# Kernel tuning notes

Hardware: AMD Instinct MI355X
Metric: run time of the kernel (lower is better)

## Reference

```python
import jax, jax.numpy as jnp
import numpy as np

B, N, IN_DIM, OUT_DIM, K = 64, 256, 512, 512, 8
DK = OUT_DIM // K  # per-kernel feature dim


def setup_inputs() -> dict:
    key = jax.random.key(0)
    k1, k2, k3, k4 = jax.random.split(key, 4)
    node_feats = jax.random.normal(k1, (B, N, IN_DIM), dtype=jnp.float32)
    adj = jax.random.uniform(k2, (B, K, N, N), dtype=jnp.float32)
    weight = jax.random.normal(k3, (IN_DIM, OUT_DIM), dtype=jnp.float32) * (1.0 / np.sqrt(IN_DIM))
    bias = jax.random.normal(k4, (OUT_DIM,), dtype=jnp.float32) * 0.01
    return {"node_feats": node_feats, "adj": adj, "weight": weight, "bias": bias}


def reference(node_feats, adj, weight, bias):
    # kernel linear + ReLU: (b, n, out_dim)
    h = jax.nn.relu(jnp.einsum('bni,io->bno', node_feats, weight) + bias)
    # split into kernel slots: (b, n, k, dk)
    h = h.reshape(B, N, K, DK)
    # graph.aggregate: per-kernel dense message passing over adjacency
    # out[b,n,k,d] = sum_m adj[b,k,n,m] * h[b,m,k,d]
    agg = jnp.einsum('bknm,bmkd->bnkd', adj, h)
    return agg.reshape(B, N, OUT_DIM)
```

## Files before the change

### kernel.cpp

```cpp
#include <hip/hip_runtime.h>
#include <hip/hip_bf16.h>


typedef __attribute__((ext_vector_type(8))) short short8;
typedef __attribute__((ext_vector_type(4))) float floatx4;

__device__ __forceinline__ unsigned short f2bf(float f) {
    union { float f; unsigned u; } v; v.f = f;
    unsigned r = v.u + 0x7FFFu + ((v.u >> 16) & 1u);
    return (unsigned short)(r >> 16);
}

__global__ __launch_bounds__(256) void wt_kernel(const float* __restrict__ W,
                                                 unsigned short* __restrict__ Wt) {
    int idx = blockIdx.x * 256 + threadIdx.x;
    int k = idx >> 9;
    int o = idx & 511;
    Wt[o * 512 + k] = f2bf(W[idx]);
}

__global__ __launch_bounds__(256) void gemm_relu_kernel(
    const float* __restrict__ X, const unsigned short* __restrict__ Wt,
    const float* __restrict__ bias, unsigned short* __restrict__ hT) {
    __shared__ unsigned short a_lds[128 * 40];
    __shared__ unsigned short b_lds[128 * 40];

    const int tid = threadIdx.x;
    const int lane = tid & 63, wid = tid >> 6;
    const int wm = (wid & 1) * 64, wn = (wid >> 1) * 64;
    const int lrow = lane & 15, quad = lane >> 4;
    const int m_base = blockIdx.x * 128;
    const int o_base = blockIdx.y * 128;

    floatx4 acc[4][4];
    const floatx4 fzero = {0.f, 0.f, 0.f, 0.f};
#pragma unroll
    for (int i = 0; i < 4; ++i)
#pragma unroll
        for (int j = 0; j < 4; ++j) acc[i][j] = fzero;

    for (int kb = 0; kb < 16; ++kb) {
        const int k0 = kb * 32;
#pragma unroll
        for (int i = 0; i < 4; ++i) {
            int c4 = tid + i * 256;
            int r = c4 >> 3;
            int cc = (c4 & 7) * 4;
            const float4 v = *(const float4*)(X + (size_t)(m_base + r) * 512 + k0 + cc);
            ushort4 p;
            p.x = f2bf(v.x); p.y = f2bf(v.y); p.z = f2bf(v.z); p.w = f2bf(v.w);
            *(ushort4*)(a_lds + r * 40 + cc) = p;
        }
#pragma unroll
        for (int i = 0; i < 4; ++i) {
            int c4 = tid + i * 256;
            int r = c4 >> 3;
            int cc = (c4 & 7) * 4;
            *(ushort4*)(b_lds + r * 40 + cc) =
                *(const ushort4*)(Wt + (size_t)(o_base + r) * 512 + k0 + cc);
        }
        __syncthreads();

        short8 af[4], bfr[4];
#pragma unroll
        for (int i = 0; i < 4; ++i)
            af[i] = *(const short8*)(a_lds + (wm + 16 * i + lrow) * 40 + quad * 8);
#pragma unroll
        for (int j = 0; j < 4; ++j)
            bfr[j] = *(const short8*)(b_lds + (wn + 16 * j + lrow) * 40 + quad * 8);
#pragma unroll
        for (int i = 0; i < 4; ++i)
#pragma unroll
            for (int j = 0; j < 4; ++j)
                acc[i][j] = __builtin_amdgcn_mfma_f32_16x16x32_bf16(af[i], bfr[j], acc[i][j], 0, 0, 0);
        __syncthreads();
    }

    const int b = blockIdx.x >> 1;
    const int m_in_b = (blockIdx.x & 1) * 128;
#pragma unroll
    for (int j = 0; j < 4; ++j) {
        int o = o_base + wn + 16 * j + lrow;
        float bv = bias[o];
        int ks = o >> 6, d = o & 63;
        unsigned short* dst = hT + ((size_t)(b * 8 + ks) * 64 + d) * 256;
#pragma unroll
        for (int i = 0; i < 4; ++i) {
            int m = m_in_b + wm + 16 * i + quad * 4;
            floatx4 c = acc[i][j];
            ushort4 p;
            p.x = f2bf(fmaxf(c.x + bv, 0.f));
            p.y = f2bf(fmaxf(c.y + bv, 0.f));
            p.z = f2bf(fmaxf(c.z + bv, 0.f));
            p.w = f2bf(fmaxf(c.w + bv, 0.f));
            *(ushort4*)(dst + m) = p;
        }
    }
}

__global__ __launch_bounds__(256) void agg_kernel(const float* __restrict__ adj,
                                                  const unsigned short* __restrict__ hT,
                                                  float* __restrict__ out) {
    const int tid = threadIdx.x;
    const int lane = tid & 63, wid = tid >> 6;
    const int bk = blockIdx.x >> 1;
    const int half = blockIdx.x & 1;
    const int b = bk >> 3, ks = bk & 7;
    const int lrow = lane & 15, quad = lane >> 4;
    const int n0 = half * 128 + wid * 32;

    const float* A = adj + (size_t)bk * 65536;
    const unsigned short* Bh = hT + (size_t)bk * 16384;

    floatx4 acc[2][4];
    const floatx4 fzero = {0.f, 0.f, 0.f, 0.f};
#pragma unroll
    for (int i = 0; i < 2; ++i)
#pragma unroll
        for (int j = 0; j < 4; ++j) acc[i][j] = fzero;

    for (int mt = 0; mt < 8; ++mt) {
        const int m0 = mt * 32 + quad * 8;
        short8 af[2], bfr[4];
#pragma unroll
        for (int i = 0; i < 2; ++i) {
            const float* src = A + (size_t)(n0 + 16 * i + lrow) * 256 + m0;
            float4 v0 = *(const float4*)src;
            float4 v1 = *(const float4*)(src + 4);
            short8 t;
            t[0] = (short)f2bf(v0.x); t[1] = (short)f2bf(v0.y);
            t[2] = (short)f2bf(v0.z); t[3] = (short)f2bf(v0.w);
            t[4] = (short)f2bf(v1.x); t[5] = (short)f2bf(v1.y);
            t[6] = (short)f2bf(v1.z); t[7] = (short)f2bf(v1.w);
            af[i] = t;
        }
#pragma unroll
        for (int j = 0; j < 4; ++j)
            bfr[j] = *(const short8*)(Bh + (16 * j + lrow) * 256 + m0);
#pragma unroll
        for (int i = 0; i < 2; ++i)
#pragma unroll
            for (int j = 0; j < 4; ++j)
                acc[i][j] = __builtin_amdgcn_mfma_f32_16x16x32_bf16(af[i], bfr[j], acc[i][j], 0, 0, 0);
    }

#pragma unroll
    for (int i = 0; i < 2; ++i) {
#pragma unroll
        for (int j = 0; j < 4; ++j) {
            int n = n0 + 16 * i + quad * 4;
            int d = 16 * j + lrow;
            float* dst = out + ((size_t)b * 256 + n) * 512 + ks * 64 + d;
            floatx4 c = acc[i][j];
            dst[0 * 512] = c.x;
            dst[1 * 512] = c.y;
            dst[2 * 512] = c.z;
            dst[3 * 512] = c.w;
        }
    }
}

extern "C" void kernel_launch(void* const* d_in, const int* in_sizes, int n_in,
                              void* d_out, int out_size, void* d_ws, size_t ws_size,
                              hipStream_t stream) {
    const float* X    = (const float*)d_in[0];
    const float* adj  = (const float*)d_in[1];
    const float* W    = (const float*)d_in[2];
    const float* bias = (const float*)d_in[3];
    float* out = (float*)d_out;

    unsigned short* hT = (unsigned short*)d_ws;
    unsigned short* Wt = hT + (size_t)64 * 8 * 64 * 256;

    wt_kernel<<<1024, 256, 0, stream>>>(W, Wt);
    gemm_relu_kernel<<<dim3(128, 4), 256, 0, stream>>>(X, Wt, bias, hT);
    agg_kernel<<<1024, 256, 0, stream>>>(adj, hT, out);
}
```

Measured before the change: 260.6 us.

## Tile weight transpose via LDS, use packed bf16 conversion, remap block order

The weight transpose kernel now stages 64x64 tiles through padded shared memory, so both its global reads and its writes are coalesced. Float-to-bf16 conversion switches to the packed __float22bfloat162_rn intrinsic in all kernels. The gemm and agg kernels remap block IDs so that consecutive groups of eight blocks take different m-tiles or bk slices, which changes how work spreads across XCDs and caches. The agg kernel reads a large fp32 adjacency tensor and likely dominates runtime, so these changes mostly touch the smaller stages.

```diff
diff --git a/kernel.cpp b/kernel.cpp
--- a/kernel.cpp
+++ b/kernel.cpp
@@ -11,12 +11,32 @@
     return (unsigned short)(r >> 16);
 }
 
+__device__ __forceinline__ unsigned pk2bf(float a, float b) {
+    union { __hip_bfloat162 h; unsigned u; } cv;
+    cv.h = __float22bfloat162_rn(make_float2(a, b));
+    return cv.u;
+}
+
 __global__ __launch_bounds__(256) void wt_kernel(const float* __restrict__ W,
                                                  unsigned short* __restrict__ Wt) {
-    int idx = blockIdx.x * 256 + threadIdx.x;
-    int k = idx >> 9;
-    int o = idx & 511;
-    Wt[o * 512 + k] = f2bf(W[idx]);
+    __shared__ unsigned short t_lds[64 * 66];
+    const int tile = blockIdx.x;
+    const int k0 = (tile >> 3) * 64;
+    const int o0 = (tile & 7) * 64;
+    const int t = threadIdx.x;
+    const int c = t & 63;
+    const int rb = t >> 6;
+#pragma unroll
+    for (int i = 0; i < 16; ++i) {
+        int r = i * 4 + rb;
+        t_lds[c * 66 + r] = f2bf(W[(size_t)(k0 + r) * 512 + o0 + c]);
+    }
+    __syncthreads();
+#pragma unroll
+    for (int i = 0; i < 16; ++i) {
+        int o_r = i * 4 + rb;
+        Wt[(size_t)(o0 + o_r) * 512 + k0 + c] = t_lds[o_r * 66 + c];
+    }
 }
 
 __global__ __launch_bounds__(256) void gemm_relu_kernel(
@@ -25,12 +45,18 @@
     __shared__ unsigned short a_lds[128 * 40];
     __shared__ unsigned short b_lds[128 * 40];
 
+    const int id = blockIdx.x;
+    const int r8 = id & 7;
+    const int yt = (id >> 3) & 3;
+    const int q  = id >> 5;
+    const int m_tile = r8 + 8 * q;
+    const int m_base = m_tile * 128;
+    const int o_base = yt * 128;
+
     const int tid = threadIdx.x;
     const int lane = tid & 63, wid = tid >> 6;
     const int wm = (wid & 1) * 64, wn = (wid >> 1) * 64;
     const int lrow = lane & 15, quad = lane >> 4;
-    const int m_base = blockIdx.x * 128;
-    const int o_base = blockIdx.y * 128;
 
     floatx4 acc[4][4];
     const floatx4 fzero = {0.f, 0.f, 0.f, 0.f};
@@ -44,20 +70,21 @@
 #pragma unroll
         for (int i = 0; i < 4; ++i) {
             int c4 = tid + i * 256;
-            int r = c4 >> 3;
+            int rr = c4 >> 3;
             int cc = (c4 & 7) * 4;
-            const float4 v = *(const float4*)(X + (size_t)(m_base + r) * 512 + k0 + cc);
-            ushort4 p;
-            p.x = f2bf(v.x); p.y = f2bf(v.y); p.z = f2bf(v.z); p.w = f2bf(v.w);
-            *(ushort4*)(a_lds + r * 40 + cc) = p;
+            const float4 v = *(const float4*)(X + (size_t)(m_base + rr) * 512 + k0 + cc);
+            unsigned p01 = pk2bf(v.x, v.y);
+            unsigned p23 = pk2bf(v.z, v.w);
+            unsigned* dst = (unsigned*)(a_lds + rr * 40 + cc);
+            dst[0] = p01; dst[1] = p23;
         }
 #pragma unroll
         for (int i = 0; i < 4; ++i) {
             int c4 = tid + i * 256;
-            int r = c4 >> 3;
+            int rr = c4 >> 3;
             int cc = (c4 & 7) * 4;
-            *(ushort4*)(b_lds + r * 40 + cc) =
-                *(const ushort4*)(Wt + (size_t)(o_base + r) * 512 + k0 + cc);
+            *(ushort4*)(b_lds + rr * 40 + cc) =
+                *(const ushort4*)(Wt + (size_t)(o_base + rr) * 512 + k0 + cc);
         }
         __syncthreads();
 
@@ -76,8 +103,8 @@
         __syncthreads();
     }
 
-    const int b = blockIdx.x >> 1;
-    const int m_in_b = (blockIdx.x & 1) * 128;
+    const int b = m_tile >> 1;
+    const int m_in_b = (m_tile & 1) * 128;
 #pragma unroll
     for (int j = 0; j < 4; ++j) {
         int o = o_base + wn + 16 * j + lrow;
@@ -88,12 +115,10 @@
         for (int i = 0; i < 4; ++i) {
             int m = m_in_b + wm + 16 * i + quad * 4;
             floatx4 c = acc[i][j];
-            ushort4 p;
-            p.x = f2bf(fmaxf(c.x + bv, 0.f));
-            p.y = f2bf(fmaxf(c.y + bv, 0.f));
-            p.z = f2bf(fmaxf(c.z + bv, 0.f));
-            p.w = f2bf(fmaxf(c.w + bv, 0.f));
-            *(ushort4*)(dst + m) = p;
+            unsigned p01 = pk2bf(fmaxf(c.x + bv, 0.f), fmaxf(c.y + bv, 0.f));
+            unsigned p23 = pk2bf(fmaxf(c.z + bv, 0.f), fmaxf(c.w + bv, 0.f));
+            unsigned* d32 = (unsigned*)(dst + m);
+            d32[0] = p01; d32[1] = p23;
         }
     }
 }
@@ -101,10 +126,14 @@
 __global__ __launch_bounds__(256) void agg_kernel(const float* __restrict__ adj,
                                                   const unsigned short* __restrict__ hT,
                                                   float* __restrict__ out) {
+    const int id = blockIdx.x;
+    const int r8 = id & 7;
+    const int half = (id >> 3) & 1;
+    const int q = id >> 4;
+    const int bk = r8 + 8 * q;
+
     const int tid = threadIdx.x;
     const int lane = tid & 63, wid = tid >> 6;
-    const int bk = blockIdx.x >> 1;
-    const int half = blockIdx.x & 1;
     const int b = bk >> 3, ks = bk & 7;
     const int lrow = lane & 15, quad = lane >> 4;
     const int n0 = half * 128 + wid * 32;
@@ -127,12 +156,12 @@
             const float* src = A + (size_t)(n0 + 16 * i + lrow) * 256 + m0;
             float4 v0 = *(const float4*)src;
             float4 v1 = *(const float4*)(src + 4);
-            short8 t;
-            t[0] = (short)f2bf(v0.x); t[1] = (short)f2bf(v0.y);
-            t[2] = (short)f2bf(v0.z); t[3] = (short)f2bf(v0.w);
-            t[4] = (short)f2bf(v1.x); t[5] = (short)f2bf(v1.y);
-            t[6] = (short)f2bf(v1.z); t[7] = (short)f2bf(v1.w);
-            af[i] = t;
+            union { short8 s; unsigned u[4]; } t;
+            t.u[0] = pk2bf(v0.x, v0.y);
+            t.u[1] = pk2bf(v0.z, v0.w);
+            t.u[2] = pk2bf(v1.x, v1.y);
+            t.u[3] = pk2bf(v1.z, v1.w);
+            af[i] = t.s;
         }
 #pragma unroll
         for (int j = 0; j < 4; ++j)
@@ -172,7 +201,7 @@
     unsigned short* hT = (unsigned short*)d_ws;
     unsigned short* Wt = hT + (size_t)64 * 8 * 64 * 256;
 
-    wt_kernel<<<1024, 256, 0, stream>>>(W, Wt);
-    gemm_relu_kernel<<<dim3(128, 4), 256, 0, stream>>>(X, Wt, bias, hT);
+    wt_kernel<<<64, 256, 0, stream>>>(W, Wt);
+    gemm_relu_kernel<<<512, 256, 0, stream>>>(X, Wt, bias, hT);
     agg_kernel<<<1024, 256, 0, stream>>>(adj, hT, out);
 }
```

Measured after the change: 255.2 us. -2.1%, faster.
